# Kernel tuning notes

Measured on AMD Instinct MI355X. Metric: run time of the kernel, lower is better.

Reference implementation:

```python
import jax, jax.numpy as jnp
import numpy as np

B, N, C = 8, 196, 512
NC, H = 10, 8
HD = C // H
SCALE = HD ** -0.5


def setup_inputs() -> dict:
    key = jax.random.key(0)
    ks = jax.random.split(key, 8)
    s = 1.0 / np.sqrt(C)
    return {
        "x": jax.random.normal(ks[0], (B, N, C), jnp.float32),
        "anchors": jax.random.normal(ks[1], (NC, N, C), jnp.float32),
        "weights": jax.random.uniform(ks[2], (B, H, NC), jnp.float32),
        "Wqk": jax.random.normal(ks[3], (C, C), jnp.float32) * s,
        "Wqk2": jax.random.normal(ks[4], (C, C), jnp.float32) * s,
        "Wv": jax.random.normal(ks[5], (C, C), jnp.float32) * s,
        "Wproj": jax.random.normal(ks[6], (C, C), jnp.float32) * s,
        "bproj": jax.random.normal(ks[7], (C,), jnp.float32) * 0.01,
    }


def _heads(t):
    # (..., N, C) -> (..., H, N, HD)
    shp = t.shape[:-2]
    return t.reshape(shp + (t.shape[-2], H, HD)).swapaxes(-3, -2)


def reference(x, anchors, weights, Wqk, Wqk2, Wv, Wproj, bproj):
    v = _heads(x @ Wv)                      # (B, H, N, HD)
    q = _heads(x @ Wqk)[:, None]            # (B, 1, H, N, HD)
    k = _heads(anchors @ Wqk)[None]         # (1, NC, H, N, HD)
    q2 = _heads(x @ Wqk2)[:, None]          # (B, 1, H, N, HD)
    k2 = _heads(anchors @ Wqk2)[None]       # (1, NC, H, N, HD)

    # ReLU-clipped double attention, both (B, NC, H, N, N)
    left_attn = jnp.maximum(-(q @ k.swapaxes(-2, -1)) * SCALE, 0.0)
    right_attn = jnp.maximum((k2 @ q2.swapaxes(-2, -1)) * SCALE, 0.0)

    attn = left_attn @ right_attn           # (B, NC, H, N, N)
    # per-head class-weighted combine: (B,H,NC) x (B,NC,H,N,N) -> (B,H,N,N)
    tmp = jnp.einsum('bhc,bchnm->bhnm', weights, attn)
    out = tmp @ v                           # (B, H, N, HD)
    # NOTE: original torch code reshapes (B,H,N,HD)->(B,N,C) WITHOUT a
    # transpose back; we replicate that exact flatten order.
    out = out.reshape(B, N, C)
    out = out @ Wproj + bproj
    return (out, left_attn)
```

## Files before the change

### kernel.cpp

```cpp
#include <hip/hip_runtime.h>

#define OFF_XQ   0u
#define OFF_XQ2  1605632u
#define OFF_XV   3211264u
#define OFF_AQ   4816896u
#define OFF_AQ2  6823936u
#define OFF_RVT  8830976u
#define OFF_P    29802496u
#define OFF_OUT1 45858816u

typedef __attribute__((ext_vector_type(8))) short bf16x8;
typedef __attribute__((ext_vector_type(4))) float f32x4;
#define MFMA(a, b, c) __builtin_amdgcn_mfma_f32_16x16x32_bf16((a), (b), (c), 0, 0, 0)

__device__ __forceinline__ unsigned short f2bf(float x) {
  unsigned u = __builtin_bit_cast(unsigned, x);
  u += 0x7fffu + ((u >> 16) & 1u);
  return (unsigned short)(u >> 16);
}
__device__ __forceinline__ float bf2f(unsigned short s) {
  return __builtin_bit_cast(float, ((unsigned)s) << 16);
}

__device__ __forceinline__ void load_bf16_tile(unsigned short T[64][72], const unsigned short* __restrict__ g,
                                               int row0, int nrows, int col0, int tid) {
  int r = tid >> 2;
  int c0 = (tid & 3) << 4;
  uint4 a = make_uint4(0, 0, 0, 0), b = make_uint4(0, 0, 0, 0);
  if (r < nrows) {
    const unsigned short* p = g + (size_t)(row0 + r) * 512 + col0 + c0;
    a = *(const uint4*)p;
    b = *(const uint4*)(p + 8);
  }
  *(uint4*)&T[r][c0] = a;
  *(uint4*)&T[r][c0 + 8] = b;
}

__device__ __forceinline__ void load_bf16_tile_T(unsigned short T[64][72], const unsigned short* __restrict__ g,
                                                 int row0, int nrows, int col0, int tid) {
#pragma unroll
  for (int rep = 0; rep < 2; rep++) {
    int j = (tid >> 3) + (rep << 5);
    int d0 = (tid & 7) << 3;
    uint4 a = make_uint4(0, 0, 0, 0);
    if (j < nrows) a = *(const uint4*)(g + (size_t)(row0 + j) * 512 + col0 + d0);
    unsigned short s[8];
    *(uint4*)s = a;
#pragma unroll
    for (int u = 0; u < 8; u++) T[d0 + u][j] = s[u];
  }
}

template <bool STORE_BF16>
__device__ __forceinline__ void gemm_mfma_body(const float* __restrict__ A, const float* __restrict__ W,
                                               const float* __restrict__ bias, void* __restrict__ outp,
                                               int M, int row_blk, int col_blk) {
  __shared__ unsigned short As[64][72];
  __shared__ unsigned short Wt[64][72];
  int row0 = row_blk << 6;
  if (row0 >= M) return;
  int col0 = col_blk << 6;
  int tid = threadIdx.x;
  int w = tid >> 6, lm = tid & 15, lq = (tid >> 4) & 3;
  f32x4 acc[4] = {};
  for (int k0 = 0; k0 < 512; k0 += 64) {
    {
      int r = tid >> 2, c0 = (tid & 3) << 4;
      float4 f0, f1, f2, f3;
      if (row0 + r < M) {
        const float* p = A + (size_t)(row0 + r) * 512 + k0 + c0;
        f0 = *(const float4*)p;       f1 = *(const float4*)(p + 4);
        f2 = *(const float4*)(p + 8); f3 = *(const float4*)(p + 12);
      } else {
        f0 = f1 = f2 = f3 = make_float4(0.f, 0.f, 0.f, 0.f);
      }
      unsigned short s[16];
      s[0] = f2bf(f0.x);  s[1] = f2bf(f0.y);  s[2] = f2bf(f0.z);  s[3] = f2bf(f0.w);
      s[4] = f2bf(f1.x);  s[5] = f2bf(f1.y);  s[6] = f2bf(f1.z);  s[7] = f2bf(f1.w);
      s[8] = f2bf(f2.x);  s[9] = f2bf(f2.y);  s[10] = f2bf(f2.z); s[11] = f2bf(f2.w);
      s[12] = f2bf(f3.x); s[13] = f2bf(f3.y); s[14] = f2bf(f3.z); s[15] = f2bf(f3.w);
      *(uint4*)&As[r][c0] = *(uint4*)s;
      *(uint4*)&As[r][c0 + 8] = *(uint4*)(s + 8);
    }
#pragma unroll
    for (int rep = 0; rep < 2; rep++) {
      int k = (tid >> 3) + (rep << 5);
      int n0 = (tid & 7) << 3;
      const float* p = W + (size_t)(k0 + k) * 512 + col0 + n0;
      float4 g0 = *(const float4*)p, g1 = *(const float4*)(p + 4);
      Wt[n0 + 0][k] = f2bf(g0.x); Wt[n0 + 1][k] = f2bf(g0.y);
      Wt[n0 + 2][k] = f2bf(g0.z); Wt[n0 + 3][k] = f2bf(g0.w);
      Wt[n0 + 4][k] = f2bf(g1.x); Wt[n0 + 5][k] = f2bf(g1.y);
      Wt[n0 + 6][k] = f2bf(g1.z); Wt[n0 + 7][k] = f2bf(g1.w);
    }
    __syncthreads();
#pragma unroll
    for (int kk = 0; kk < 2; kk++) {
      bf16x8 bf = *(const bf16x8*)&Wt[(w << 4) + lm][(kk << 5) + (lq << 3)];
#pragma unroll
      for (int mi = 0; mi < 4; mi++) {
        bf16x8 af = *(const bf16x8*)&As[(mi << 4) + lm][(kk << 5) + (lq << 3)];
        acc[mi] = MFMA(af, bf, acc[mi]);
      }
    }
    __syncthreads();
  }
  int ncol = col0 + (w << 4) + lm;
  float bv = bias ? bias[ncol] : 0.f;
#pragma unroll
  for (int mi = 0; mi < 4; mi++)
#pragma unroll
    for (int r2 = 0; r2 < 4; r2++) {
      int row = row0 + (mi << 4) + (lq << 2) + r2;
      if (row < M) {
        if (STORE_BF16)
          ((unsigned short*)outp)[(size_t)row * 512 + ncol] = f2bf(acc[mi][r2]);
        else
          ((float*)outp)[(size_t)row * 512 + ncol] = acc[mi][r2] + bv;
      }
    }
}

__global__ __launch_bounds__(256) void proj5(const float* __restrict__ x, const float* __restrict__ anchors,
                                             const float* __restrict__ Wqk, const float* __restrict__ Wqk2,
                                             const float* __restrict__ Wv, char* __restrict__ ws) {
  const float* A; const float* W; unsigned short* O; int M;
  switch (blockIdx.z) {
    case 0:  A = x;       W = Wqk;  O = (unsigned short*)(ws + OFF_XQ);  M = 1568; break;
    case 1:  A = x;       W = Wqk2; O = (unsigned short*)(ws + OFF_XQ2); M = 1568; break;
    case 2:  A = x;       W = Wv;   O = (unsigned short*)(ws + OFF_XV);  M = 1568; break;
    case 3:  A = anchors; W = Wqk;  O = (unsigned short*)(ws + OFF_AQ);  M = 1960; break;
    default: A = anchors; W = Wqk2; O = (unsigned short*)(ws + OFF_AQ2); M = 1960; break;
  }
  gemm_mfma_body<true>(A, W, nullptr, O, M, blockIdx.x, blockIdx.y);
}

__global__ __launch_bounds__(256) void final_gemm(const float* __restrict__ A, const float* __restrict__ W,
                                                  const float* __restrict__ bias, float* __restrict__ out) {
  gemm_mfma_body<false>(A, W, bias, out, 1568, blockIdx.x, blockIdx.y);
}

__global__ __launch_bounds__(256) void rv_mfma(const unsigned short* __restrict__ xq2,
                                               const unsigned short* __restrict__ aq2,
                                               const unsigned short* __restrict__ xv,
                                               unsigned short* __restrict__ rvt) {
  __shared__ unsigned short Ks[64][72];
  __shared__ unsigned short Qs[64][72];
  __shared__ unsigned short Vt[64][72];
  __shared__ unsigned short Ss[64][72];
  int i0 = blockIdx.x << 6;
  int bch = blockIdx.y;
  int h = bch & 7, bc = bch >> 3;
  int c = bc % 10, b = bc / 10;
  int tid = threadIdx.x;
  int w = tid >> 6, lm = tid & 15, lq = (tid >> 4) & 3;
  int ni = min(64, 196 - i0);

  load_bf16_tile(Ks, aq2, c * 196 + i0, ni, h << 6, tid);
  __syncthreads();
  bf16x8 kf[4][2];
#pragma unroll
  for (int mi = 0; mi < 4; mi++)
#pragma unroll
    for (int kk = 0; kk < 2; kk++)
      kf[mi][kk] = *(const bf16x8*)&Ks[(mi << 4) + lm][(kk << 5) + (lq << 3)];

  f32x4 acc[4] = {};
  for (int jt = 0; jt < 4; jt++) {
    int j0 = jt << 6;
    int nj = min(64, 196 - j0);
    __syncthreads();
    load_bf16_tile(Qs, xq2, b * 196 + j0, nj, h << 6, tid);
    load_bf16_tile_T(Vt, xv, b * 196 + j0, nj, h << 6, tid);
    __syncthreads();
    f32x4 s[4] = {};
#pragma unroll
    for (int kk = 0; kk < 2; kk++) {
      bf16x8 bf = *(const bf16x8*)&Qs[(w << 4) + lm][(kk << 5) + (lq << 3)];
#pragma unroll
      for (int mi = 0; mi < 4; mi++) s[mi] = MFMA(kf[mi][kk], bf, s[mi]);
    }
#pragma unroll
    for (int mi = 0; mi < 4; mi++)
#pragma unroll
      for (int r = 0; r < 4; r++)
        Ss[(mi << 4) + (lq << 2) + r][(w << 4) + lm] = f2bf(fmaxf(0.125f * s[mi][r], 0.f));
    __syncthreads();
#pragma unroll
    for (int kk = 0; kk < 2; kk++) {
      bf16x8 bf = *(const bf16x8*)&Vt[(w << 4) + lm][(kk << 5) + (lq << 3)];
#pragma unroll
      for (int mi = 0; mi < 4; mi++) {
        bf16x8 af = *(const bf16x8*)&Ss[(mi << 4) + lm][(kk << 5) + (lq << 3)];
        acc[mi] = MFMA(af, bf, acc[mi]);
      }
    }
  }
  __syncthreads();
#pragma unroll
  for (int mi = 0; mi < 4; mi++)
#pragma unroll
    for (int r = 0; r < 4; r++)
      Ss[(w << 4) + lm][(mi << 4) + (lq << 2) + r] = f2bf(acc[mi][r]);
  __syncthreads();
  {
    int dd = tid >> 2, seg = (tid & 3) << 4;
    unsigned short* dst = rvt + ((size_t)bch * 64 + dd) * 256 + i0 + seg;
    *(uint4*)dst = *(uint4*)&Ss[dd][seg];
    *(uint4*)(dst + 8) = *(uint4*)&Ss[dd][seg + 8];
  }
}

__global__ __launch_bounds__(256) void attn_mfma(const unsigned short* __restrict__ xq,
                                                 const unsigned short* __restrict__ aq,
                                                 const unsigned short* __restrict__ rvt,
                                                 float* __restrict__ left,
                                                 unsigned short* __restrict__ P) {
  __shared__ unsigned short Qs[64][72];
  __shared__ unsigned short Ks[64][72];
  __shared__ unsigned short Rt[64][72];
  __shared__ unsigned short Ss[64][72];
  int i0 = blockIdx.x << 6;
  int bh = blockIdx.y;
  int c = blockIdx.z;
  int b = bh >> 3, h = bh & 7;
  int bch = (b * 10 + c) * 8 + h;
  int tid = threadIdx.x;
  int w = tid >> 6, lm = tid & 15, lq = (tid >> 4) & 3;
  int ni = min(64, 196 - i0);

  load_bf16_tile(Qs, xq, b * 196 + i0, ni, h << 6, tid);
  __syncthreads();
  bf16x8 qf[4][2];
#pragma unroll
  for (int mi = 0; mi < 4; mi++)
#pragma unroll
    for (int kk = 0; kk < 2; kk++)
      qf[mi][kk] = *(const bf16x8*)&Qs[(mi << 4) + lm][(kk << 5) + (lq << 3)];

  f32x4 acc[4] = {};
  size_t lbase = (size_t)bch * (196 * 196);
  for (int jt = 0; jt < 4; jt++) {
    int j0 = jt << 6;
    int nj = min(64, 196 - j0);
    __syncthreads();
    load_bf16_tile(Ks, aq, c * 196 + j0, nj, h << 6, tid);
    {
      int dd = tid >> 2, seg = (tid & 3) << 4;
      const unsigned short* src = rvt + ((size_t)bch * 64 + dd) * 256 + j0 + seg;
      *(uint4*)&Rt[dd][seg] = *(const uint4*)src;
      *(uint4*)&Rt[dd][seg + 8] = *(const uint4*)(src + 8);
    }
    __syncthreads();
    f32x4 s[4] = {};
#pragma unroll
    for (int kk = 0; kk < 2; kk++) {
      bf16x8 bf = *(const bf16x8*)&Ks[(w << 4) + lm][(kk << 5) + (lq << 3)];
#pragma unroll
      for (int mi = 0; mi < 4; mi++) s[mi] = MFMA(qf[mi][kk], bf, s[mi]);
    }
#pragma unroll
    for (int mi = 0; mi < 4; mi++)
#pragma unroll
      for (int r = 0; r < 4; r++) {
        float v = fmaxf(-0.125f * s[mi][r], 0.f);
        int il = (mi << 4) + (lq << 2) + r;
        int jl = (w << 4) + lm;
        Ss[il][jl] = f2bf(v);
        if (i0 + il < 196 && j0 + jl < 196)
          left[lbase + (size_t)(i0 + il) * 196 + (j0 + jl)] = v;
      }
    __syncthreads();
#pragma unroll
    for (int kk = 0; kk < 2; kk++) {
      bf16x8 bf = *(const bf16x8*)&Rt[(w << 4) + lm][(kk << 5) + (lq << 3)];
#pragma unroll
      for (int mi = 0; mi < 4; mi++) {
        bf16x8 af = *(const bf16x8*)&Ss[(mi << 4) + lm][(kk << 5) + (lq << 3)];
        acc[mi] = MFMA(af, bf, acc[mi]);
      }
    }
  }
  __syncthreads();
#pragma unroll
  for (int mi = 0; mi < 4; mi++)
#pragma unroll
    for (int r = 0; r < 4; r++)
      Ss[(mi << 4) + (lq << 2) + r][(w << 4) + lm] = f2bf(acc[mi][r]);
  __syncthreads();
  {
    int row = tid >> 2, seg = (tid & 3) << 4;
    if (i0 + row < 196) {
      unsigned short* dst = P + ((size_t)(bh * 10 + c) * 196 + i0 + row) * 64 + seg;
      *(uint4*)dst = *(uint4*)&Ss[row][seg];
      *(uint4*)(dst + 8) = *(uint4*)&Ss[row][seg + 8];
    }
  }
}

__global__ __launch_bounds__(256) void reduce_out1(const unsigned short* __restrict__ P,
                                                   const float* __restrict__ weights,
                                                   float* __restrict__ out1) {
  int t = blockIdx.x * 256 + threadIdx.x;
  int base = t << 2;
  int bh = base / 12544;
  int rem = base - bh * 12544;
  const float* wrow = weights + bh * 10;
  float a0 = 0.f, a1 = 0.f, a2 = 0.f, a3 = 0.f;
#pragma unroll
  for (int c = 0; c < 10; c++) {
    float wc = wrow[c];
    const unsigned short* p = P + ((size_t)(bh * 10 + c)) * 12544 + rem;
    ushort4 u = *(const ushort4*)p;
    a0 = fmaf(wc, bf2f(u.x), a0);
    a1 = fmaf(wc, bf2f(u.y), a1);
    a2 = fmaf(wc, bf2f(u.z), a2);
    a3 = fmaf(wc, bf2f(u.w), a3);
  }
  *(float4*)&out1[base] = make_float4(a0, a1, a2, a3);
}

extern "C" void kernel_launch(void* const* d_in, const int* in_sizes, int n_in,
                              void* d_out, int out_size, void* d_ws, size_t ws_size,
                              hipStream_t stream) {
  (void)in_sizes; (void)n_in; (void)out_size; (void)ws_size;
  const float* x       = (const float*)d_in[0];
  const float* anchors = (const float*)d_in[1];
  const float* weights = (const float*)d_in[2];
  const float* Wqk     = (const float*)d_in[3];
  const float* Wqk2    = (const float*)d_in[4];
  const float* Wv      = (const float*)d_in[5];
  const float* Wproj   = (const float*)d_in[6];
  const float* bproj   = (const float*)d_in[7];
  char* ws = (char*)d_ws;
  float* out  = (float*)d_out;
  float* left = out + 802816;

  unsigned short* xq  = (unsigned short*)(ws + OFF_XQ);
  unsigned short* xq2 = (unsigned short*)(ws + OFF_XQ2);
  unsigned short* xv  = (unsigned short*)(ws + OFF_XV);
  unsigned short* aq  = (unsigned short*)(ws + OFF_AQ);
  unsigned short* aq2 = (unsigned short*)(ws + OFF_AQ2);
  unsigned short* rvt = (unsigned short*)(ws + OFF_RVT);
  unsigned short* P   = (unsigned short*)(ws + OFF_P);
  float* out1         = (float*)(ws + OFF_OUT1);

  dim3 blk(256);
  proj5<<<dim3(31, 8, 5), blk, 0, stream>>>(x, anchors, Wqk, Wqk2, Wv, ws);
  rv_mfma<<<dim3(4, 640), blk, 0, stream>>>(xq2, aq2, xv, rvt);
  attn_mfma<<<dim3(4, 64, 10), blk, 0, stream>>>(xq, aq, rvt, left, P);
  reduce_out1<<<dim3(784), blk, 0, stream>>>(P, weights, out1);
  final_gemm<<<dim3(25, 8), blk, 0, stream>>>(out1, Wproj, bproj, out);
}
```

Measured before the change: 242.7 us.

## Pre-convert inputs to bf16 and stage tiles with direct global-to-LDS loads

Adds a pre-pass that converts x and anchors to bf16 and writes pre-transposed bf16 copies of all weight matrices. The GEMMs and attention kernels then stage tiles with global_load_lds DMA instead of per-thread loads, conversions and scattered transposed LDS writes. The rvt layout is retiled into contiguous 64x64 blocks, the attention loop handles the ragged last tile first with a zeroed LDS region, and out1 is stored as bf16. This removes repeated fp32-to-bf16 conversion and strided transposes from every GEMM block, at the cost of an extra kernel launch, extra workspace traffic, and lower precision on the final projection input.

```diff
diff --git a/kernel.cpp b/kernel.cpp
--- a/kernel.cpp
+++ b/kernel.cpp
@@ -1,13 +1,19 @@
 #include <hip/hip_runtime.h>
 
-#define OFF_XQ   0u
-#define OFF_XQ2  1605632u
-#define OFF_XV   3211264u
-#define OFF_AQ   4816896u
-#define OFF_AQ2  6823936u
-#define OFF_RVT  8830976u
-#define OFF_P    29802496u
-#define OFF_OUT1 45858816u
+#define OFF_XB     0u
+#define OFF_AB     1605632u
+#define OFF_WQKT   3612672u
+#define OFF_WQK2T  4136960u
+#define OFF_WVT    4661248u
+#define OFF_WPROJT 5185536u
+#define OFF_XQ     5709824u
+#define OFF_XQ2    7315456u
+#define OFF_XV     8921088u
+#define OFF_AQ     10526720u
+#define OFF_AQ2    12533760u
+#define OFF_RVT    14540800u
+#define OFF_OUT1   35512320u
+#define OFF_P      37117952u
 
 typedef __attribute__((ext_vector_type(8))) short bf16x8;
 typedef __attribute__((ext_vector_type(4))) float f32x4;
@@ -20,6 +26,31 @@
 }
 __device__ __forceinline__ float bf2f(unsigned short s) {
   return __builtin_bit_cast(float, ((unsigned)s) << 16);
+}
+
+__device__ __forceinline__ void gl_lds16(const void* g, void* l) {
+  __builtin_amdgcn_global_load_lds(
+      (const __attribute__((address_space(1))) unsigned int*)g,
+      (__attribute__((address_space(3))) unsigned int*)l, 16, 0, 0);
+}
+
+__device__ __forceinline__ void stage64(const unsigned short* g0, int stride,
+                                        unsigned short (*T)[72], int tid, int nrows) {
+  int wv = tid >> 6;
+  char* base = (char*)&T[0][0];
+#pragma unroll
+  for (int i = 0; i < 2; i++) {
+    int k = i * 256 + tid;
+    int r = k / 9, c = k - r * 9;
+    if (r < nrows)
+      gl_lds16(g0 + (size_t)r * stride + (c << 3), base + (((i << 2) + wv) << 10));
+  }
+  if (tid < 64) {
+    int k = 512 + tid;
+    int r = k / 9, c = k - r * 9;
+    if (r < nrows)
+      gl_lds16(g0 + (size_t)r * stride + (c << 3), base + 8192);
+  }
 }
 
 __device__ __forceinline__ void load_bf16_tile(unsigned short T[64][72], const unsigned short* __restrict__ g,
@@ -51,12 +82,62 @@
   }
 }
 
+__global__ __launch_bounds__(256) void pre_kernel(const float* __restrict__ x, const float* __restrict__ anchors,
+                                                  const float* __restrict__ Wqk, const float* __restrict__ Wqk2,
+                                                  const float* __restrict__ Wv, const float* __restrict__ Wproj,
+                                                  char* __restrict__ ws) {
+  int tid = threadIdx.x;
+  if (blockIdx.x < 1764) {
+    int base = blockIdx.x * 1024 + (tid << 2);
+    float4 f = (base < 802816) ? *(const float4*)(x + base)
+                               : *(const float4*)(anchors + (base - 802816));
+    unsigned short s[4] = {f2bf(f.x), f2bf(f.y), f2bf(f.z), f2bf(f.w)};
+    *(uint2*)((unsigned short*)(ws + OFF_XB) + base) = *(uint2*)s;
+    return;
+  }
+  __shared__ unsigned short Ls[64][72];
+  int idx = blockIdx.x - 1764;
+  int wsel = idx >> 6, t = idx & 63;
+  int k0 = (t >> 3) << 6, n0 = (t & 7) << 6;
+  const float* W;
+  unsigned short* WT;
+  switch (wsel) {
+    case 0:  W = Wqk;   WT = (unsigned short*)(ws + OFF_WQKT);   break;
+    case 1:  W = Wqk2;  WT = (unsigned short*)(ws + OFF_WQK2T);  break;
+    case 2:  W = Wv;    WT = (unsigned short*)(ws + OFF_WVT);    break;
+    default: W = Wproj; WT = (unsigned short*)(ws + OFF_WPROJT); break;
+  }
+  {
+    int r = tid >> 2, seg = (tid & 3) << 4;
+    const float* p = W + (size_t)(k0 + r) * 512 + n0 + seg;
+    float4 f0 = *(const float4*)p, f1 = *(const float4*)(p + 4);
+    float4 f2 = *(const float4*)(p + 8), f3 = *(const float4*)(p + 12);
+    unsigned short s[16] = {f2bf(f0.x), f2bf(f0.y), f2bf(f0.z), f2bf(f0.w),
+                            f2bf(f1.x), f2bf(f1.y), f2bf(f1.z), f2bf(f1.w),
+                            f2bf(f2.x), f2bf(f2.y), f2bf(f2.z), f2bf(f2.w),
+                            f2bf(f3.x), f2bf(f3.y), f2bf(f3.z), f2bf(f3.w)};
+    *(uint4*)&Ls[r][seg] = *(uint4*)s;
+    *(uint4*)&Ls[r][seg + 8] = *(uint4*)(s + 8);
+  }
+  __syncthreads();
+  {
+    int r = tid >> 2, seg = (tid & 3) << 4;
+    unsigned short s[16];
+#pragma unroll
+    for (int u = 0; u < 16; u++) s[u] = Ls[seg + u][r];
+    unsigned short* dst = WT + (size_t)(n0 + r) * 512 + k0 + seg;
+    *(uint4*)dst = *(uint4*)s;
+    *(uint4*)(dst + 8) = *(uint4*)(s + 8);
+  }
+}
+
 template <bool STORE_BF16>
-__device__ __forceinline__ void gemm_mfma_body(const float* __restrict__ A, const float* __restrict__ W,
+__device__ __forceinline__ void gemm_bf16_body(const unsigned short* __restrict__ A,
+                                               const unsigned short* __restrict__ WT,
                                                const float* __restrict__ bias, void* __restrict__ outp,
                                                int M, int row_blk, int col_blk) {
   __shared__ unsigned short As[64][72];
-  __shared__ unsigned short Wt[64][72];
+  __shared__ unsigned short Ws[64][72];
   int row0 = row_blk << 6;
   if (row0 >= M) return;
   int col0 = col_blk << 6;
@@ -64,46 +145,19 @@
   int w = tid >> 6, lm = tid & 15, lq = (tid >> 4) & 3;
   f32x4 acc[4] = {};
   for (int k0 = 0; k0 < 512; k0 += 64) {
-    {
-      int r = tid >> 2, c0 = (tid & 3) << 4;
-      float4 f0, f1, f2, f3;
-      if (row0 + r < M) {
-        const float* p = A + (size_t)(row0 + r) * 512 + k0 + c0;
-        f0 = *(const float4*)p;       f1 = *(const float4*)(p + 4);
-        f2 = *(const float4*)(p + 8); f3 = *(const float4*)(p + 12);
-      } else {
-        f0 = f1 = f2 = f3 = make_float4(0.f, 0.f, 0.f, 0.f);
-      }
-      unsigned short s[16];
-      s[0] = f2bf(f0.x);  s[1] = f2bf(f0.y);  s[2] = f2bf(f0.z);  s[3] = f2bf(f0.w);
-      s[4] = f2bf(f1.x);  s[5] = f2bf(f1.y);  s[6] = f2bf(f1.z);  s[7] = f2bf(f1.w);
-      s[8] = f2bf(f2.x);  s[9] = f2bf(f2.y);  s[10] = f2bf(f2.z); s[11] = f2bf(f2.w);
-      s[12] = f2bf(f3.x); s[13] = f2bf(f3.y); s[14] = f2bf(f3.z); s[15] = f2bf(f3.w);
-      *(uint4*)&As[r][c0] = *(uint4*)s;
-      *(uint4*)&As[r][c0 + 8] = *(uint4*)(s + 8);
-    }
-#pragma unroll
-    for (int rep = 0; rep < 2; rep++) {
-      int k = (tid >> 3) + (rep << 5);
-      int n0 = (tid & 7) << 3;
-      const float* p = W + (size_t)(k0 + k) * 512 + col0 + n0;
-      float4 g0 = *(const float4*)p, g1 = *(const float4*)(p + 4);
-      Wt[n0 + 0][k] = f2bf(g0.x); Wt[n0 + 1][k] = f2bf(g0.y);
-      Wt[n0 + 2][k] = f2bf(g0.z); Wt[n0 + 3][k] = f2bf(g0.w);
-      Wt[n0 + 4][k] = f2bf(g1.x); Wt[n0 + 5][k] = f2bf(g1.y);
-      Wt[n0 + 6][k] = f2bf(g1.z); Wt[n0 + 7][k] = f2bf(g1.w);
-    }
+    __syncthreads();
+    stage64(A + (size_t)row0 * 512 + k0, 512, As, tid, 64);
+    stage64(WT + (size_t)col0 * 512 + k0, 512, Ws, tid, 64);
     __syncthreads();
 #pragma unroll
     for (int kk = 0; kk < 2; kk++) {
-      bf16x8 bf = *(const bf16x8*)&Wt[(w << 4) + lm][(kk << 5) + (lq << 3)];
+      bf16x8 bf = *(const bf16x8*)&Ws[(w << 4) + lm][(kk << 5) + (lq << 3)];
 #pragma unroll
       for (int mi = 0; mi < 4; mi++) {
         bf16x8 af = *(const bf16x8*)&As[(mi << 4) + lm][(kk << 5) + (lq << 3)];
         acc[mi] = MFMA(af, bf, acc[mi]);
       }
     }
-    __syncthreads();
   }
   int ncol = col0 + (w << 4) + lm;
   float bv = bias ? bias[ncol] : 0.f;
@@ -121,29 +175,31 @@
     }
 }
 
-__global__ __launch_bounds__(256) void proj5(const float* __restrict__ x, const float* __restrict__ anchors,
-                                             const float* __restrict__ Wqk, const float* __restrict__ Wqk2,
-                                             const float* __restrict__ Wv, char* __restrict__ ws) {
-  const float* A; const float* W; unsigned short* O; int M;
+__global__ __launch_bounds__(256) void proj5(char* __restrict__ ws) {
+  const unsigned short* xb = (const unsigned short*)(ws + OFF_XB);
+  const unsigned short* ab = (const unsigned short*)(ws + OFF_AB);
+  const unsigned short* A; const unsigned short* WT; unsigned short* O; int M;
   switch (blockIdx.z) {
-    case 0:  A = x;       W = Wqk;  O = (unsigned short*)(ws + OFF_XQ);  M = 1568; break;
-    case 1:  A = x;       W = Wqk2; O = (unsigned short*)(ws + OFF_XQ2); M = 1568; break;
-    case 2:  A = x;       W = Wv;   O = (unsigned short*)(ws + OFF_XV);  M = 1568; break;
-    case 3:  A = anchors; W = Wqk;  O = (unsigned short*)(ws + OFF_AQ);  M = 1960; break;
-    default: A = anchors; W = Wqk2; O = (unsigned short*)(ws + OFF_AQ2); M = 1960; break;
-  }
-  gemm_mfma_body<true>(A, W, nullptr, O, M, blockIdx.x, blockIdx.y);
-}
-
-__global__ __launch_bounds__(256) void final_gemm(const float* __restrict__ A, const float* __restrict__ W,
+    case 0:  A = xb; WT = (unsigned short*)(ws + OFF_WQKT);  O = (unsigned short*)(ws + OFF_XQ);  M = 1568; break;
+    case 1:  A = xb; WT = (unsigned short*)(ws + OFF_WQK2T); O = (unsigned short*)(ws + OFF_XQ2); M = 1568; break;
+    case 2:  A = xb; WT = (unsigned short*)(ws + OFF_WVT);   O = (unsigned short*)(ws + OFF_XV);  M = 1568; break;
+    case 3:  A = ab; WT = (unsigned short*)(ws + OFF_WQKT);  O = (unsigned short*)(ws + OFF_AQ);  M = 1960; break;
+    default: A = ab; WT = (unsigned short*)(ws + OFF_WQK2T); O = (unsigned short*)(ws + OFF_AQ2); M = 1960; break;
+  }
+  gemm_bf16_body<true>(A, WT, nullptr, O, M, blockIdx.x, blockIdx.y);
+}
+
+__global__ __launch_bounds__(256) void final_gemm(const unsigned short* __restrict__ out1,
+                                                  const unsigned short* __restrict__ WT,
                                                   const float* __restrict__ bias, float* __restrict__ out) {
-  gemm_mfma_body<false>(A, W, bias, out, 1568, blockIdx.x, blockIdx.y);
-}
-
-__global__ __launch_bounds__(256) void rv_mfma(const unsigned short* __restrict__ xq2,
-                                               const unsigned short* __restrict__ aq2,
-                                               const unsigned short* __restrict__ xv,
-                                               unsigned short* __restrict__ rvt) {
+  gemm_bf16_body<false>(out1, WT, bias, out, 1568, blockIdx.x, blockIdx.y);
+}
+
+__global__ __launch_bounds__(256) void rv_mfma(char* __restrict__ ws) {
+  const unsigned short* xq2 = (const unsigned short*)(ws + OFF_XQ2);
+  const unsigned short* aq2 = (const unsigned short*)(ws + OFF_AQ2);
+  const unsigned short* xv  = (const unsigned short*)(ws + OFF_XV);
+  unsigned short* rvt       = (unsigned short*)(ws + OFF_RVT);
   __shared__ unsigned short Ks[64][72];
   __shared__ unsigned short Qs[64][72];
   __shared__ unsigned short Vt[64][72];
@@ -170,7 +226,7 @@
     int j0 = jt << 6;
     int nj = min(64, 196 - j0);
     __syncthreads();
-    load_bf16_tile(Qs, xq2, b * 196 + j0, nj, h << 6, tid);
+    stage64(xq2 + (size_t)(b * 196 + j0) * 512 + (h << 6), 512, Qs, tid, 64);
     load_bf16_tile_T(Vt, xv, b * 196 + j0, nj, h << 6, tid);
     __syncthreads();
     f32x4 s[4] = {};
@@ -205,17 +261,17 @@
   __syncthreads();
   {
     int dd = tid >> 2, seg = (tid & 3) << 4;
-    unsigned short* dst = rvt + ((size_t)bch * 64 + dd) * 256 + i0 + seg;
+    unsigned short* dst = rvt + ((size_t)(bch * 4 + blockIdx.x) * 64 + dd) * 64 + seg;
     *(uint4*)dst = *(uint4*)&Ss[dd][seg];
     *(uint4*)(dst + 8) = *(uint4*)&Ss[dd][seg + 8];
   }
 }
 
-__global__ __launch_bounds__(256) void attn_mfma(const unsigned short* __restrict__ xq,
-                                                 const unsigned short* __restrict__ aq,
-                                                 const unsigned short* __restrict__ rvt,
-                                                 float* __restrict__ left,
+__global__ __launch_bounds__(256) void attn_mfma(char* __restrict__ ws, float* __restrict__ left,
                                                  unsigned short* __restrict__ P) {
+  const unsigned short* xq  = (const unsigned short*)(ws + OFF_XQ);
+  const unsigned short* aq  = (const unsigned short*)(ws + OFF_AQ);
+  const unsigned short* rvt = (const unsigned short*)(ws + OFF_RVT);
   __shared__ unsigned short Qs[64][72];
   __shared__ unsigned short Ks[64][72];
   __shared__ unsigned short Rt[64][72];
@@ -227,31 +283,32 @@
   int bch = (b * 10 + c) * 8 + h;
   int tid = threadIdx.x;
   int w = tid >> 6, lm = tid & 15, lq = (tid >> 4) & 3;
-  int ni = min(64, 196 - i0);
-
-  load_bf16_tile(Qs, xq, b * 196 + i0, ni, h << 6, tid);
-  __syncthreads();
+
+  stage64(xq + (size_t)(b * 196 + i0) * 512 + (h << 6), 512, Qs, tid, 64);
   bf16x8 qf[4][2];
-#pragma unroll
-  for (int mi = 0; mi < 4; mi++)
-#pragma unroll
-    for (int kk = 0; kk < 2; kk++)
-      qf[mi][kk] = *(const bf16x8*)&Qs[(mi << 4) + lm][(kk << 5) + (lq << 3)];
-
   f32x4 acc[4] = {};
   size_t lbase = (size_t)bch * (196 * 196);
-  for (int jt = 0; jt < 4; jt++) {
+#pragma unroll
+  for (int t = 0; t < 4; t++) {
+    int jt = (t == 0) ? 3 : t - 1;
     int j0 = jt << 6;
-    int nj = min(64, 196 - j0);
-    __syncthreads();
-    load_bf16_tile(Ks, aq, c * 196 + j0, nj, h << 6, tid);
-    {
-      int dd = tid >> 2, seg = (tid & 3) << 4;
-      const unsigned short* src = rvt + ((size_t)bch * 64 + dd) * 256 + j0 + seg;
-      *(uint4*)&Rt[dd][seg] = *(const uint4*)src;
-      *(uint4*)&Rt[dd][seg + 8] = *(const uint4*)(src + 8);
-    }
-    __syncthreads();
+    int nj = (jt == 3) ? 4 : 64;
+    __syncthreads();
+    if (t == 0) {
+      uint4 z = make_uint4(0, 0, 0, 0);
+      for (int k = tid; k < 540; k += 256)
+        *(uint4*)((char*)&Ks[0][0] + 576 + k * 16) = z;
+    }
+    stage64(aq + (size_t)(c * 196 + j0) * 512 + (h << 6), 512, Ks, tid, nj);
+    stage64(rvt + (size_t)(bch * 4 + jt) * 4096, 64, Rt, tid, 64);
+    __syncthreads();
+    if (t == 0) {
+#pragma unroll
+      for (int mi = 0; mi < 4; mi++)
+#pragma unroll
+        for (int kk = 0; kk < 2; kk++)
+          qf[mi][kk] = *(const bf16x8*)&Qs[(mi << 4) + lm][(kk << 5) + (lq << 3)];
+    }
     f32x4 s[4] = {};
 #pragma unroll
     for (int kk = 0; kk < 2; kk++) {
@@ -300,7 +357,7 @@
 
 __global__ __launch_bounds__(256) void reduce_out1(const unsigned short* __restrict__ P,
                                                    const float* __restrict__ weights,
-                                                   float* __restrict__ out1) {
+                                                   unsigned short* __restrict__ out1) {
   int t = blockIdx.x * 256 + threadIdx.x;
   int base = t << 2;
   int bh = base / 12544;
@@ -317,7 +374,8 @@
     a2 = fmaf(wc, bf2f(u.z), a2);
     a3 = fmaf(wc, bf2f(u.w), a3);
   }
-  *(float4*)&out1[base] = make_float4(a0, a1, a2, a3);
+  unsigned short s[4] = {f2bf(a0), f2bf(a1), f2bf(a2), f2bf(a3)};
+  *(uint2*)&out1[base] = *(uint2*)s;
 }
 
 extern "C" void kernel_launch(void* const* d_in, const int* in_sizes, int n_in,
@@ -336,19 +394,13 @@
   float* out  = (float*)d_out;
   float* left = out + 802816;
 
-  unsigned short* xq  = (unsigned short*)(ws + OFF_XQ);
-  unsigned short* xq2 = (unsigned short*)(ws + OFF_XQ2);
-  unsigned short* xv  = (unsigned short*)(ws + OFF_XV);
-  unsigned short* aq  = (unsigned short*)(ws + OFF_AQ);
-  unsigned short* aq2 = (unsigned short*)(ws + OFF_AQ2);
-  unsigned short* rvt = (unsigned short*)(ws + OFF_RVT);
-  unsigned short* P   = (unsigned short*)(ws + OFF_P);
-  float* out1         = (float*)(ws + OFF_OUT1);
-
   dim3 blk(256);
-  proj5<<<dim3(31, 8, 5), blk, 0, stream>>>(x, anchors, Wqk, Wqk2, Wv, ws);
-  rv_mfma<<<dim3(4, 640), blk, 0, stream>>>(xq2, aq2, xv, rvt);
-  attn_mfma<<<dim3(4, 64, 10), blk, 0, stream>>>(xq, aq, rvt, left, P);
-  reduce_out1<<<dim3(784), blk, 0, stream>>>(P, weights, out1);
-  final_gemm<<<dim3(25, 8), blk, 0, stream>>>(out1, Wproj, bproj, out);
-}
+  pre_kernel<<<dim3(2020), blk, 0, stream>>>(x, anchors, Wqk, Wqk2, Wv, Wproj, ws);
+  proj5<<<dim3(31, 8, 5), blk, 0, stream>>>(ws);
+  rv_mfma<<<dim3(4, 640), blk, 0, stream>>>(ws);
+  attn_mfma<<<dim3(4, 64, 10), blk, 0, stream>>>(ws, left, (unsigned short*)(ws + OFF_P));
+  reduce_out1<<<dim3(784), blk, 0, stream>>>((const unsigned short*)(ws + OFF_P), weights,
+                                             (unsigned short*)(ws + OFF_OUT1));
+  final_gemm<<<dim3(25, 8), blk, 0, stream>>>((const unsigned short*)(ws + OFF_OUT1),
+                                              (const unsigned short*)(ws + OFF_WPROJT), bproj, out);
+}
```

After: 230.4 us. 1.05x faster.
